# Kernel tuning notes

Hardware: AMD Instinct MI355X
Metric: run time of the kernel (lower is better)

## Reference

```python
import jax, jax.numpy as jnp
import numpy as np
from jax import lax

CIN, COUT, K, PAD = 256, 128, 3, 1


def setup_inputs() -> dict:
    key = jax.random.key(0)
    ks = jax.random.split(key, 5)
    N, h0, w0 = 2, 64, 64
    x = jax.random.normal(ks[0], (N, CIN, h0, w0), jnp.float32)
    lateral_feat = jax.random.normal(ks[1], (N, COUT, 1, 1), jnp.float32)
    trans_w = jax.random.normal(ks[2], (CIN, COUT, K, K), jnp.float32) * 0.02
    off_w1 = jax.random.normal(ks[3], (64, COUT, 3, 3), jnp.float32) * 0.02
    off_b1 = jnp.zeros((64,), jnp.float32)
    off_w2 = jax.random.normal(ks[4], (2 * K * K, 64, 3, 3), jnp.float32) * 0.02
    off_b2 = jnp.zeros((2 * K * K,), jnp.float32)
    return dict(x=x, lateral_feat=lateral_feat, trans_w=trans_w,
                off_w1=off_w1, off_b1=off_b1, off_w2=off_w2, off_b2=off_b2)


def _conv2d(x, w, b, pad):
    y = lax.conv_general_dilated(x, w, (1, 1), [(pad, pad), (pad, pad)],
                                 dimension_numbers=('NCHW', 'OIHW', 'NCHW'))
    return y + b[None, :, None, None]


def _conv_transpose2d(x, w, stride, pad, out_pad):
    # torch ConvTranspose2d weight layout: [Cin, Cout, k, k]
    k = w.shape[2]
    wt = jnp.flip(w, (2, 3)).transpose(1, 0, 2, 3)  # [Cout, Cin, k, k]
    lo = k - 1 - pad
    hi = k - 1 - pad + out_pad
    return lax.conv_general_dilated(x, wt, (1, 1), [(lo, hi), (lo, hi)],
                                    lhs_dilation=(stride, stride),
                                    dimension_numbers=('NCHW', 'OIHW', 'NCHW'))


def _deform_conv2d(x, offset, w, pad):
    # x [N,C,H,W], offset [N,2*K*K,H,W] (y,x interleaved per kernel tap), w [O,C,K,K]
    N, C, H, W = x.shape
    O = w.shape[0]
    KK = K * K
    off = offset.reshape(N, KK, 2, H, W)
    ky = jnp.arange(KK) // K
    kx = jnp.arange(KK) % K
    py = jnp.arange(H)[None, None, :, None] + (ky - pad)[None, :, None, None] + off[:, :, 0]
    px = jnp.arange(W)[None, None, None, :] + (kx - pad)[None, :, None, None] + off[:, :, 1]
    y0 = jnp.floor(py)
    x0 = jnp.floor(px)
    dy = py - y0
    dx = px - x0
    y0i = y0.astype(jnp.int32)
    x0i = x0.astype(jnp.int32)
    xf = x.reshape(N, C, H * W)

    def corner(yi, xi, wgt):
        valid = (yi >= 0) & (yi < H) & (xi >= 0) & (xi < W)
        idx = (jnp.clip(yi, 0, H - 1) * W + jnp.clip(xi, 0, W - 1)).reshape(N, -1)
        v = jnp.take_along_axis(xf, idx[:, None, :], axis=2).reshape(N, C, KK, H, W)
        return v * (wgt * valid)[:, None]

    sampled = (corner(y0i, x0i, (1 - dy) * (1 - dx))
               + corner(y0i, x0i + 1, (1 - dy) * dx)
               + corner(y0i + 1, x0i, dy * (1 - dx))
               + corner(y0i + 1, x0i + 1, dy * dx))  # [N,C,KK,H,W]
    return jnp.einsum('nckhw,ock->nohw', sampled, w.reshape(O, C, KK))


def reference(x, lateral_feat, trans_w, off_w1, off_b1, off_w2, off_b2):
    up = _conv_transpose2d(x, trans_w, 2, PAD, 1)          # [N, COUT, 2h0, 2w0]
    h = jax.nn.relu(_conv2d(lateral_feat, off_w1, off_b1, 1))
    offset = jnp.tanh(_conv2d(h, off_w2, off_b2, 1))       # [N, 18, 1, 1]
    N, C, H, W = up.shape
    # offset.repeat(1, 1, H, W) with 1x1 spatial input == broadcast to full grid
    offset = jnp.broadcast_to(offset, (N, 2 * K * K, H, W))
    # deform_conv2d uses trans_conv weight [O=CIN, I=COUT, K, K], stride=1, pad=PAD
    return _deform_conv2d(up, offset, trans_w, PAD)        # [N, CIN, H, W]
```

## Files before the change

### kernel.cpp

```cpp
#include <hip/hip_runtime.h>
#include <hip/hip_bf16.h>
#include <math.h>

typedef __attribute__((ext_vector_type(8))) short s16x8;
typedef __attribute__((ext_vector_type(4))) float f32x4;
typedef __attribute__((ext_vector_type(2))) float v2f;

__device__ __forceinline__ unsigned short f2bf(float f) {
    union { float f; unsigned int u; } v; v.f = f;
    unsigned int u = v.u + 0x7FFFu + ((v.u >> 16) & 1u);
    return (unsigned short)(u >> 16);
}
__device__ __forceinline__ unsigned pk2(float lo, float hi) {
    __hip_bfloat162 h = __float22bfloat162_rn(make_float2(lo, hi));
    union { __hip_bfloat162 h; unsigned u; } v; v.h = h;
    return v.u;
}
__device__ __forceinline__ v2f up2(unsigned u) {
    union { unsigned u; float f; } a, b;
    a.u = u << 16; b.u = u & 0xffff0000u;
    v2f r; r.x = a.f; r.y = b.f; return r;
}

__device__ __forceinline__ void blend4(uint4 uA, uint4 uB, uint4 uC, uint4 uD,
                                       v2f c00, v2f c01, v2f c10, v2f c11,
                                       unsigned short* dst) {
    unsigned ua[4] = {uA.x, uA.y, uA.z, uA.w};
    unsigned ub[4] = {uB.x, uB.y, uB.z, uB.w};
    unsigned uc[4] = {uC.x, uC.y, uC.z, uC.w};
    unsigned ud[4] = {uD.x, uD.y, uD.z, uD.w};
    unsigned pk[4];
#pragma unroll
    for (int i = 0; i < 4; ++i) {
        v2f r = c00 * up2(ua[i]) + c01 * up2(ub[i]) + c10 * up2(uc[i]) + c11 * up2(ud[i]);
        pk[i] = pk2(r.x, r.y);
    }
    *(uint4*)dst = make_uint4(pk[0], pk[1], pk[2], pk[3]);
}

__global__ __launch_bounds__(256) void k_prep(const float* __restrict__ x,
                                              const float* __restrict__ lat,
                                              const float* __restrict__ tw,
                                              const float* __restrict__ w1,
                                              const float* __restrict__ b1,
                                              const float* __restrict__ w2,
                                              const float* __restrict__ b2,
                                              unsigned short* __restrict__ xp,
                                              unsigned short* __restrict__ A2f,
                                              unsigned short* __restrict__ Awf,
                                              int* __restrict__ ipar,
                                              float* __restrict__ fpar) {
    __shared__ float sm[8420];
    int b = blockIdx.x, t = threadIdx.x;
    if (b == 0) {
        for (int i = t; i < 8192; i += 256) sm[(i >> 7) * 129 + (i & 127)] = w1[i * 9 + 4];
        __syncthreads();
        if (t < 128) {
            int n = t >> 6, o = t & 63;
            float s = b1[o];
            const float* ln = lat + n * 128;
#pragma unroll 8
            for (int c = 0; c < 128; ++c) s += ln[c] * sm[o * 129 + c];
            sm[8256 + t] = fmaxf(s, 0.f);
        }
        __syncthreads();
        if (t < 36) {
            int n = t / 18, j = t % 18;
            float s = b2[j];
            for (int o = 0; o < 64; ++o) s += sm[8256 + n * 64 + o] * w2[(j * 64 + o) * 9 + 4];
            float ov = tanhf(s);
            ov = fminf(fmaxf(ov, -0.999999f), 0.999999f);
            sm[8384 + t] = ov;
        }
        __syncthreads();
        if (t < 36) {
            int n = t / 18, j = t % 18;
            int tap = j >> 1, d = j & 1;
            float ov = sm[8384 + t];
            float fl = floorf(ov);
            int kc = d ? (tap % 3) : (tap / 3);
            ipar[(n * 9 + tap) * 2 + d] = kc - 1 + (int)fl;
            fpar[(n * 9 + tap) * 2 + d] = ov - fl;
        }
    } else if (b < 145) {
        int slot = (b - 1) * 256 + t;
        int l = slot & 63;
        int mi = (slot >> 6) & 3;
        int w = (slot >> 8) & 3;
        int k = slot >> 10;
        int row = w * 64 + mi * 16 + (l & 15);
        int kq = l >> 4;
        unsigned short v[8];
#pragma unroll
        for (int j = 0; j < 8; ++j) {
            int kcol = k * 32 + kq * 8 + j;
            int tap = kcol >> 7, c = kcol & 127;
            v[j] = f2bf(tw[(row * 128 + c) * 9 + tap]);
        }
        unsigned p0 = (unsigned)v[0] | ((unsigned)v[1] << 16);
        unsigned p1 = (unsigned)v[2] | ((unsigned)v[3] << 16);
        unsigned p2 = (unsigned)v[4] | ((unsigned)v[5] << 16);
        unsigned p3 = (unsigned)v[6] | ((unsigned)v[7] << 16);
        *(uint4*)(A2f + slot * 8) = make_uint4(p0, p1, p2, p3);
    } else if (b < 289) {
        int slot = (b - 145) * 256 + t;
        int l = slot & 63;
        int mi = (slot >> 6) & 3;
        int wm = (slot >> 8) & 1;
        int k = slot >> 9;
        int row = wm * 64 + mi * 16 + (l & 15);
        int kq = l >> 4;
        unsigned short v[8];
#pragma unroll
        for (int j = 0; j < 8; ++j) {
            int kcol = k * 32 + kq * 8 + j;
            int t9 = kcol >> 8, ci = kcol & 255;
            int ky = t9 / 3, kx = t9 - ky * 3;
            v[j] = f2bf(tw[(ci * 128 + row) * 9 + (2 - ky) * 3 + (2 - kx)]);
        }
        unsigned p0 = (unsigned)v[0] | ((unsigned)v[1] << 16);
        unsigned p1 = (unsigned)v[2] | ((unsigned)v[3] << 16);
        unsigned p2 = (unsigned)v[4] | ((unsigned)v[5] << 16);
        unsigned p3 = (unsigned)v[6] | ((unsigned)v[7] << 16);
        *(uint4*)(Awf + slot * 8) = make_uint4(p0, p1, p2, p3);
    } else {
        int bb = b - 289;
        int h = bb & 63, cq = (bb >> 6) & 3, n = bb >> 8;
        int c0 = cq * 64;
        {
            int wcol = t & 63, sub = t >> 6;
            for (int r = 0; r < 16; ++r) {
                int ci_l = r * 4 + sub;
                sm[ci_l * 65 + wcol] = x[((n * 256 + c0 + ci_l) * 64 + h) * 64 + wcol];
            }
        }
        __syncthreads();
        int wcol = t >> 2, cg = t & 3;
        unsigned short* dst = xp + (size_t)n * (65 * 65 * 256) + (h * 65 + wcol) * 256 + c0 + cg * 16;
        unsigned pk[8];
#pragma unroll
        for (int j = 0; j < 8; ++j)
            pk[j] = pk2(sm[(cg * 16 + 2 * j) * 65 + wcol], sm[(cg * 16 + 2 * j + 1) * 65 + wcol]);
        *(uint4*)dst = make_uint4(pk[0], pk[1], pk[2], pk[3]);
        *(uint4*)(dst + 8) = make_uint4(pk[4], pk[5], pk[6], pk[7]);
    }
}

__global__ __launch_bounds__(256) void k_tconv4(const unsigned short* __restrict__ xp,
                                                const unsigned short* __restrict__ Awf,
                                                unsigned short* __restrict__ upp) {
    int t = threadIdx.x;
    int b = blockIdx.x;
    int cls = b >> 7;
    int phase = (cls < 2) ? 1 : 0;
    int xpar = 1 - (cls & 1);
    int idx = b & 127;
    int n = idx >> 6, yh = idx & 63;
    int y = 2 * yh + phase;
    const unsigned short* xpn = xp + (size_t)n * (65 * 65 * 256);

    int lane = t & 63, w = t >> 6;
    int col = lane & 15, q = lane >> 4;
    int pos = w * 16 + col;

    int nky = phase ? 2 : 1;
    int nkx = xpar ? 2 : 1;

    f32x4 acc[8];
#pragma unroll
    for (int mi = 0; mi < 8; ++mi) acc[mi] = (f32x4){0.f, 0.f, 0.f, 0.f};

    const unsigned short* Afl = Awf + lane * 8;

    for (int a1 = 0; a1 < nky; ++a1) {
        int ky = phase ? (a1 ? 2 : 0) : 1;
        int d2 = (y + ky - 1) >> 1;
        for (int a2 = 0; a2 < nkx; ++a2) {
            int kx = xpar ? (a2 ? 2 : 0) : 1;
            int s = (xpar + kx - 1) >> 1;
            int t9 = ky * 3 + kx;
            const unsigned short* bptr = xpn + ((size_t)(d2 * 65 + s + pos)) * 256 + q * 8;
            const unsigned short* aptr = Afl + t9 * 8 * 4096;
#pragma unroll 2
            for (int cb = 0; cb < 8; ++cb) {
                s16x8 bf = *(const s16x8*)(bptr + cb * 32);
                s16x8 a[8];
#pragma unroll
                for (int mi = 0; mi < 8; ++mi)
                    a[mi] = *(const s16x8*)(aptr + cb * 4096 + (mi >> 2) * 2048 + (mi & 3) * 512);
#pragma unroll
                for (int mi = 0; mi < 8; ++mi)
                    acc[mi] = __builtin_amdgcn_mfma_f32_16x16x32_bf16(a[mi], bf, acc[mi], 0, 0, 0);
            }
        }
    }

    unsigned short* uppn = upp + (size_t)n * (132 * 132 * 128);
    int xg = 2 * pos + xpar;
#pragma unroll
    for (int mi = 0; mi < 8; ++mi) {
        int co = mi * 16 + q * 4;
        unsigned short* p = uppn + ((y + 2) * 132 + (xg + 2)) * 128 + co;
        unsigned lo = pk2(acc[mi][0], acc[mi][1]);
        unsigned hi = pk2(acc[mi][2], acc[mi][3]);
        *(uint2*)p = make_uint2(lo, hi);
    }
}

__global__ __launch_bounds__(256, 2) void k_deform4(const unsigned short* __restrict__ upp,
                                                    const unsigned short* __restrict__ A2f,
                                                    const int* __restrict__ ipar,
                                                    const float* __restrict__ fpar,
                                                    float* __restrict__ out) {
    __shared__ unsigned short Bs[2][64][84];
    int t = threadIdx.x;
    int b = blockIdx.x;
    int xcd = b & 7, j = b >> 3;
    int n = xcd >> 2, band = xcd & 3;
    int y = band * 32 + (j & 31);
    int tx0 = (j >> 5) * 64;
    const unsigned short* uppn = upp + (size_t)n * (132 * 132 * 128);

    int lane = t & 63, w = t >> 6;
    int col = lane & 15, q = lane >> 4;
    int bx = t >> 2, bcg = t & 3;
    int boff = bx * 128 + bcg * 8;

    const int* ipn = ipar + n * 18;
    const float* fpn = fpar + n * 18;

    f32x4 acc[4][4];
#pragma unroll
    for (int mi = 0; mi < 4; ++mi)
#pragma unroll
        for (int ni = 0; ni < 4; ++ni) acc[mi][ni] = (f32x4){0.f, 0.f, 0.f, 0.f};

    const unsigned short* Afw = A2f + w * 2048 + lane * 8;

#define TAPP(tap, PB, C00, C01, C10, C11)                                        \
    {                                                                            \
        int iy = ipn[(tap)*2], ix = ipn[(tap)*2 + 1];                            \
        float fy = fpn[(tap)*2], fx = fpn[(tap)*2 + 1];                          \
        float w00 = (1.f - fy) * (1.f - fx), w01 = (1.f - fy) * fx;              \
        float w10 = fy * (1.f - fx), w11 = fy * fx;                              \
        C00 = (v2f){w00, w00}; C01 = (v2f){w01, w01};                            \
        C10 = (v2f){w10, w10}; C11 = (v2f){w11, w11};                            \
        PB = uppn + ((size_t)((y + 2 + iy) * 132 + (tx0 + 2 + ix))) * 128 + boff;\
    }

    const unsigned short* pb;
    v2f cN00, cN01, cN10, cN11;
    uint4 cr[8];
    s16x8 a_cur[8], a_nxt[8];

    TAPP(0, pb, cN00, cN01, cN10, cN11);
#pragma unroll
    for (int c = 0; c < 2; ++c) {
        const unsigned short* p = pb + c * 32;
        cr[c * 4 + 0] = *(const uint4*)p;
        cr[c * 4 + 1] = *(const uint4*)(p + 128);
        cr[c * 4 + 2] = *(const uint4*)(p + 16896);
        cr[c * 4 + 3] = *(const uint4*)(p + 17024);
    }
#pragma unroll
    for (int c = 0; c < 2; ++c)
#pragma unroll
        for (int mi = 0; mi < 4; ++mi)
            a_cur[c * 4 + mi] = *(const s16x8*)(Afw + c * 8192 + mi * 512);
#pragma unroll
    for (int c = 0; c < 2; ++c)
        blend4(cr[c * 4 + 0], cr[c * 4 + 1], cr[c * 4 + 2], cr[c * 4 + 3],
               cN00, cN01, cN10, cN11, &Bs[0][bx][c * 42 + bcg * 8]);
#pragma unroll
    for (int c = 0; c < 2; ++c) {
        const unsigned short* p = pb + 64 + c * 32;
        cr[c * 4 + 0] = *(const uint4*)p;
        cr[c * 4 + 1] = *(const uint4*)(p + 128);
        cr[c * 4 + 2] = *(const uint4*)(p + 16896);
        cr[c * 4 + 3] = *(const uint4*)(p + 17024);
    }
    __syncthreads();

#pragma unroll 2
    for (int kk = 0; kk < 18; ++kk) {
        int cur = kk & 1;
        if (kk < 17) {
#pragma unroll
            for (int c = 0; c < 2; ++c)
                blend4(cr[c * 4 + 0], cr[c * 4 + 1], cr[c * 4 + 2], cr[c * 4 + 3],
                       cN00, cN01, cN10, cN11, &Bs[cur ^ 1][bx][c * 42 + bcg * 8]);
#pragma unroll
            for (int c = 0; c < 2; ++c)
#pragma unroll
                for (int mi = 0; mi < 4; ++mi)
                    a_nxt[c * 4 + mi] = *(const s16x8*)(Afw + (size_t)(2 * (kk + 1) + c) * 8192 + mi * 512);
        }
        if (kk < 16) {
            int kk2 = kk + 2;
            TAPP(kk2 >> 1, pb, cN00, cN01, cN10, cN11);
            int cb0 = (kk2 & 1) ? 64 : 0;
#pragma unroll
            for (int c = 0; c < 2; ++c) {
                const unsigned short* p = pb + cb0 + c * 32;
                cr[c * 4 + 0] = *(const uint4*)p;
                cr[c * 4 + 1] = *(const uint4*)(p + 128);
                cr[c * 4 + 2] = *(const uint4*)(p + 16896);
                cr[c * 4 + 3] = *(const uint4*)(p + 17024);
            }
        }
#pragma unroll
        for (int c = 0; c < 2; ++c) {
            s16x8 bbf[4];
#pragma unroll
            for (int ni = 0; ni < 4; ++ni)
                bbf[ni] = *(const s16x8*)&Bs[cur][ni * 16 + col][c * 42 + q * 8];
#pragma unroll
            for (int mi = 0; mi < 4; ++mi)
#pragma unroll
                for (int ni = 0; ni < 4; ++ni)
                    acc[mi][ni] = __builtin_amdgcn_mfma_f32_16x16x32_bf16(a_cur[c * 4 + mi], bbf[ni], acc[mi][ni], 0, 0, 0);
        }
        if (kk < 17) {
#pragma unroll
            for (int i = 0; i < 8; ++i) a_cur[i] = a_nxt[i];
        }
        __syncthreads();
    }
#undef TAPP

#pragma unroll
    for (int mi = 0; mi < 4; ++mi)
#pragma unroll
        for (int ni = 0; ni < 4; ++ni) {
            int o = w * 64 + mi * 16 + q * 4;
            int xg = tx0 + ni * 16 + col;
            float* p = out + (((size_t)(n * 256 + o)) * 128 + y) * 128 + xg;
            p[0]         = acc[mi][ni][0];
            p[16384]     = acc[mi][ni][1];
            p[2 * 16384] = acc[mi][ni][2];
            p[3 * 16384] = acc[mi][ni][3];
        }
}

extern "C" void kernel_launch(void* const* d_in, const int* in_sizes, int n_in,
                              void* d_out, int out_size, void* d_ws, size_t ws_size,
                              hipStream_t stream) {
    const float* x   = (const float*)d_in[0];
    const float* lat = (const float*)d_in[1];
    const float* tw  = (const float*)d_in[2];
    const float* w1  = (const float*)d_in[3];
    const float* b1  = (const float*)d_in[4];
    const float* w2  = (const float*)d_in[5];
    const float* b2  = (const float*)d_in[6];
    float* out = (float*)d_out;

    char* ws = (char*)d_ws;
    unsigned short* upp = (unsigned short*)ws;
    unsigned short* xp  = (unsigned short*)(ws + 8921088);
    unsigned short* A2f = (unsigned short*)(ws + 13247488);
    unsigned short* Awf = (unsigned short*)(ws + 13837312);
    int*   ipar         = (int*)(ws + 14427136);
    float* fpar         = (float*)(ws + 14427424);

    hipMemsetAsync(ws, 0, 13247488, stream);
    k_prep<<<801, 256, 0, stream>>>(x, lat, tw, w1, b1, w2, b2, xp, A2f, Awf, ipar, fpar);
    k_tconv4<<<512, 256, 0, stream>>>(xp, Awf, upp);
    k_deform4<<<512, 256, 0, stream>>>(upp, A2f, ipar, fpar, out);
}
```

Baseline: 157.9 us.

## Fold bilinear deform sampling into per-shift effective weights for the deform GEMM

Because the offsets are spatially uniform, the bilinear sampling is rewritten as a sum over a small set of unique integer shifts of the upsampled map. Each shift gets an effective weight matrix built by combining the per-tap weights with the bilinear coefficients in a new k_buildA kernel. The deform kernel then becomes a plain MFMA GEMM that loads B fragments directly from global memory, with no per-block blending or shared-memory staging and a dynamic K length. This adds a kernel launch and a larger workspace, and it relies on uniform offsets, which holds for the reference semantics.

```diff
diff --git a/kernel.cpp b/kernel.cpp
--- a/kernel.cpp
+++ b/kernel.cpp
@@ -20,22 +20,6 @@
     union { unsigned u; float f; } a, b;
     a.u = u << 16; b.u = u & 0xffff0000u;
     v2f r; r.x = a.f; r.y = b.f; return r;
-}
-
-__device__ __forceinline__ void blend4(uint4 uA, uint4 uB, uint4 uC, uint4 uD,
-                                       v2f c00, v2f c01, v2f c10, v2f c11,
-                                       unsigned short* dst) {
-    unsigned ua[4] = {uA.x, uA.y, uA.z, uA.w};
-    unsigned ub[4] = {uB.x, uB.y, uB.z, uB.w};
-    unsigned uc[4] = {uC.x, uC.y, uC.z, uC.w};
-    unsigned ud[4] = {uD.x, uD.y, uD.z, uD.w};
-    unsigned pk[4];
-#pragma unroll
-    for (int i = 0; i < 4; ++i) {
-        v2f r = c00 * up2(ua[i]) + c01 * up2(ub[i]) + c10 * up2(uc[i]) + c11 * up2(ud[i]);
-        pk[i] = pk2(r.x, r.y);
-    }
-    *(uint4*)dst = make_uint4(pk[0], pk[1], pk[2], pk[3]);
 }
 
 __global__ __launch_bounds__(256) void k_prep(const float* __restrict__ x,
@@ -46,11 +30,13 @@
                                               const float* __restrict__ w2,
                                               const float* __restrict__ b2,
                                               unsigned short* __restrict__ xp,
-                                              unsigned short* __restrict__ A2f,
+                                              unsigned short* __restrict__ A2,
                                               unsigned short* __restrict__ Awf,
-                                              int* __restrict__ ipar,
-                                              float* __restrict__ fpar) {
+                                              int* __restrict__ soff_g,
+                                              int* __restrict__ nsl_g,
+                                              float* __restrict__ weff_g) {
     __shared__ float sm[8420];
+    __shared__ int ish[200];
     int b = blockIdx.x, t = threadIdx.x;
     if (b == 0) {
         for (int i = t; i < 8192; i += 256) sm[(i >> 7) * 129 + (i & 127)] = w1[i * 9 + 4];
@@ -73,35 +59,67 @@
             sm[8384 + t] = ov;
         }
         __syncthreads();
-        if (t < 36) {
-            int n = t / 18, j = t % 18;
-            int tap = j >> 1, d = j & 1;
-            float ov = sm[8384 + t];
-            float fl = floorf(ov);
-            int kc = d ? (tap % 3) : (tap / 3);
-            ipar[(n * 9 + tap) * 2 + d] = kc - 1 + (int)fl;
-            fpar[(n * 9 + tap) * 2 + d] = ov - fl;
+        if (t < 2) {
+            int n2 = t;
+            float* wl = &sm[n2 * 256];
+            int* dyA  = &ish[n2 * 100];
+            int* dxA  = dyA + 25;
+            int* keyA = dyA + 50;
+            int* mapA = dyA + 75;
+            for (int i = 0; i < 225; ++i) wl[i] = 0.f;
+            for (int i = 0; i < 25; ++i) mapA[i] = -1;
+            int ns = 0;
+            for (int tap = 0; tap < 9; ++tap) {
+                float oy = sm[8384 + n2 * 18 + 2 * tap];
+                float ox = sm[8384 + n2 * 18 + 2 * tap + 1];
+                float fly = floorf(oy), flx = floorf(ox);
+                int iy = tap / 3 - 1 + (int)fly;
+                int ix = tap % 3 - 1 + (int)flx;
+                float fy = oy - fly, fx = ox - flx;
+                for (int cr = 0; cr < 4; ++cr) {
+                    int cy = cr >> 1, cx = cr & 1;
+                    float wv = (cy ? fy : 1.f - fy) * (cx ? fx : 1.f - fx);
+                    if (wv == 0.f) continue;
+                    int dy = iy + cy, dx = ix + cx;
+                    int sid = (dy + 2) * 5 + (dx + 2);
+                    int s = mapA[sid];
+                    if (s < 0) { s = ns; mapA[sid] = s; dyA[s] = dy; dxA[s] = dx; keyA[s] = sid; ++ns; }
+                    wl[s * 9 + tap] += wv;
+                }
+            }
+            for (int a = 0; a < ns - 1; ++a) {
+                int m = a;
+                for (int bq = a + 1; bq < ns; ++bq) if (keyA[bq] < keyA[m]) m = bq;
+                if (m != a) {
+                    int tmp;
+                    tmp = keyA[a]; keyA[a] = keyA[m]; keyA[m] = tmp;
+                    tmp = dyA[a];  dyA[a]  = dyA[m];  dyA[m]  = tmp;
+                    tmp = dxA[a];  dxA[a]  = dxA[m];  dxA[m]  = tmp;
+                    for (int e = 0; e < 9; ++e) {
+                        float f = wl[a * 9 + e]; wl[a * 9 + e] = wl[m * 9 + e]; wl[m * 9 + e] = f;
+                    }
+                }
+            }
+            nsl_g[n2] = ns * 4;
+            for (int s = 0; s < ns; ++s)
+                soff_g[n2 * 32 + s] = (dyA[s] * 132 + dxA[s]) * 128;
+            for (int i = 0; i < 225; ++i) weff_g[n2 * 225 + i] = wl[i];
         }
     } else if (b < 145) {
-        int slot = (b - 1) * 256 + t;
-        int l = slot & 63;
-        int mi = (slot >> 6) & 3;
-        int w = (slot >> 8) & 3;
-        int k = slot >> 10;
-        int row = w * 64 + mi * 16 + (l & 15);
-        int kq = l >> 4;
+        int e0 = ((b - 1) * 256 + t) * 8;
+        int o = e0 / 1152, rem = e0 - o * 1152;
         unsigned short v[8];
 #pragma unroll
-        for (int j = 0; j < 8; ++j) {
-            int kcol = k * 32 + kq * 8 + j;
-            int tap = kcol >> 7, c = kcol & 127;
-            v[j] = f2bf(tw[(row * 128 + c) * 9 + tap]);
+        for (int jj = 0; jj < 8; ++jj) {
+            int kk = rem + jj;
+            int tap = kk >> 7, c = kk & 127;
+            v[jj] = f2bf(tw[(o * 128 + c) * 9 + tap]);
         }
         unsigned p0 = (unsigned)v[0] | ((unsigned)v[1] << 16);
         unsigned p1 = (unsigned)v[2] | ((unsigned)v[3] << 16);
         unsigned p2 = (unsigned)v[4] | ((unsigned)v[5] << 16);
         unsigned p3 = (unsigned)v[6] | ((unsigned)v[7] << 16);
-        *(uint4*)(A2f + slot * 8) = make_uint4(p0, p1, p2, p3);
+        *(uint4*)(A2 + e0) = make_uint4(p0, p1, p2, p3);
     } else if (b < 289) {
         int slot = (b - 145) * 256 + t;
         int l = slot & 63;
@@ -112,11 +130,11 @@
         int kq = l >> 4;
         unsigned short v[8];
 #pragma unroll
-        for (int j = 0; j < 8; ++j) {
-            int kcol = k * 32 + kq * 8 + j;
+        for (int jj = 0; jj < 8; ++jj) {
+            int kcol = k * 32 + kq * 8 + jj;
             int t9 = kcol >> 8, ci = kcol & 255;
             int ky = t9 / 3, kx = t9 - ky * 3;
-            v[j] = f2bf(tw[(ci * 128 + row) * 9 + (2 - ky) * 3 + (2 - kx)]);
+            v[jj] = f2bf(tw[(ci * 128 + row) * 9 + (2 - ky) * 3 + (2 - kx)]);
         }
         unsigned p0 = (unsigned)v[0] | ((unsigned)v[1] << 16);
         unsigned p1 = (unsigned)v[2] | ((unsigned)v[3] << 16);
@@ -139,10 +157,50 @@
         unsigned short* dst = xp + (size_t)n * (65 * 65 * 256) + (h * 65 + wcol) * 256 + c0 + cg * 16;
         unsigned pk[8];
 #pragma unroll
-        for (int j = 0; j < 8; ++j)
-            pk[j] = pk2(sm[(cg * 16 + 2 * j) * 65 + wcol], sm[(cg * 16 + 2 * j + 1) * 65 + wcol]);
+        for (int jj = 0; jj < 8; ++jj)
+            pk[jj] = pk2(sm[(cg * 16 + 2 * jj) * 65 + wcol], sm[(cg * 16 + 2 * jj + 1) * 65 + wcol]);
         *(uint4*)dst = make_uint4(pk[0], pk[1], pk[2], pk[3]);
         *(uint4*)(dst + 8) = make_uint4(pk[4], pk[5], pk[6], pk[7]);
+    }
+}
+
+__global__ __launch_bounds__(256) void k_buildA(const unsigned short* __restrict__ A2,
+                                                const float* __restrict__ weff_g,
+                                                const int* __restrict__ nsl_g,
+                                                unsigned short* __restrict__ Apf) {
+    __shared__ float wt[9];
+    int b = blockIdx.x;
+    int n = b / 100, k = b % 100;
+    if (k >= nsl_g[n]) return;
+    int s = k >> 2, cq = k & 3;
+    int t = threadIdx.x;
+    if (t < 9) wt[t] = weff_g[n * 225 + s * 9 + t];
+    __syncthreads();
+    int w = t >> 6, mi = (t >> 4) & 3, lg = t & 15;
+#pragma unroll
+    for (int i = 0; i < 4; ++i) {
+        int l = lg * 4 + i;
+        int row = w * 64 + mi * 16 + (l & 15);
+        int kq = l >> 4;
+        int c0 = cq * 32 + kq * 8;
+        const unsigned short* ap = A2 + row * 1152 + c0;
+        v2f val[4] = {(v2f){0.f,0.f},(v2f){0.f,0.f},(v2f){0.f,0.f},(v2f){0.f,0.f}};
+#pragma unroll
+        for (int tap = 0; tap < 9; ++tap) {
+            float wv = wt[tap];
+            v2f wv2 = (v2f){wv, wv};
+            uint4 u = *(const uint4*)(ap + tap * 128);
+            val[0] += wv2 * up2(u.x);
+            val[1] += wv2 * up2(u.y);
+            val[2] += wv2 * up2(u.z);
+            val[3] += wv2 * up2(u.w);
+        }
+        uint4 o4;
+        o4.x = pk2(val[0].x, val[0].y);
+        o4.y = pk2(val[1].x, val[1].y);
+        o4.z = pk2(val[2].x, val[2].y);
+        o4.w = pk2(val[3].x, val[3].y);
+        *(uint4*)(Apf + (size_t)n * 819200 + ((((k * 4 + w) * 4 + mi) * 64 + l) * 8)) = o4;
     }
 }
 
@@ -207,12 +265,11 @@
     }
 }
 
-__global__ __launch_bounds__(256, 2) void k_deform4(const unsigned short* __restrict__ upp,
-                                                    const unsigned short* __restrict__ A2f,
-                                                    const int* __restrict__ ipar,
-                                                    const float* __restrict__ fpar,
-                                                    float* __restrict__ out) {
-    __shared__ unsigned short Bs[2][64][84];
+__global__ __launch_bounds__(256) void k_deform5(const unsigned short* __restrict__ upp,
+                                                 const unsigned short* __restrict__ Apf,
+                                                 const int* __restrict__ soff_g,
+                                                 const int* __restrict__ nsl_g,
+                                                 float* __restrict__ out) {
     int t = threadIdx.x;
     int b = blockIdx.x;
     int xcd = b & 7, j = b >> 3;
@@ -223,11 +280,11 @@
 
     int lane = t & 63, w = t >> 6;
     int col = lane & 15, q = lane >> 4;
-    int bx = t >> 2, bcg = t & 3;
-    int boff = bx * 128 + bcg * 8;
-
-    const int* ipn = ipar + n * 18;
-    const float* fpn = fpar + n * 18;
+
+    int nch = nsl_g[n];
+    const int* soff = soff_g + n * 32;
+    const unsigned short* Af = Apf + (size_t)n * 819200 + w * 2048 + lane * 8;
+    int bb = ((y + 2) * 132 + (tx0 + 2)) * 128 + q * 8;
 
     f32x4 acc[4][4];
 #pragma unroll
@@ -235,98 +292,39 @@
 #pragma unroll
         for (int ni = 0; ni < 4; ++ni) acc[mi][ni] = (f32x4){0.f, 0.f, 0.f, 0.f};
 
-    const unsigned short* Afw = A2f + w * 2048 + lane * 8;
-
-#define TAPP(tap, PB, C00, C01, C10, C11)                                        \
-    {                                                                            \
-        int iy = ipn[(tap)*2], ix = ipn[(tap)*2 + 1];                            \
-        float fy = fpn[(tap)*2], fx = fpn[(tap)*2 + 1];                          \
-        float w00 = (1.f - fy) * (1.f - fx), w01 = (1.f - fy) * fx;              \
-        float w10 = fy * (1.f - fx), w11 = fy * fx;                              \
-        C00 = (v2f){w00, w00}; C01 = (v2f){w01, w01};                            \
-        C10 = (v2f){w10, w10}; C11 = (v2f){w11, w11};                            \
-        PB = uppn + ((size_t)((y + 2 + iy) * 132 + (tx0 + 2 + ix))) * 128 + boff;\
-    }
-
-    const unsigned short* pb;
-    v2f cN00, cN01, cN10, cN11;
-    uint4 cr[8];
-    s16x8 a_cur[8], a_nxt[8];
-
-    TAPP(0, pb, cN00, cN01, cN10, cN11);
-#pragma unroll
-    for (int c = 0; c < 2; ++c) {
-        const unsigned short* p = pb + c * 32;
-        cr[c * 4 + 0] = *(const uint4*)p;
-        cr[c * 4 + 1] = *(const uint4*)(p + 128);
-        cr[c * 4 + 2] = *(const uint4*)(p + 16896);
-        cr[c * 4 + 3] = *(const uint4*)(p + 17024);
-    }
-#pragma unroll
-    for (int c = 0; c < 2; ++c)
+    s16x8 a_c[4], b_c[4], a_n[4], b_n[4];
+    {
+        const unsigned short* bp = uppn + bb + soff[0];
+#pragma unroll
+        for (int ni = 0; ni < 4; ++ni)
+            b_c[ni] = *(const s16x8*)(bp + (ni * 16 + col) * 128);
 #pragma unroll
         for (int mi = 0; mi < 4; ++mi)
-            a_cur[c * 4 + mi] = *(const s16x8*)(Afw + c * 8192 + mi * 512);
-#pragma unroll
-    for (int c = 0; c < 2; ++c)
-        blend4(cr[c * 4 + 0], cr[c * 4 + 1], cr[c * 4 + 2], cr[c * 4 + 3],
-               cN00, cN01, cN10, cN11, &Bs[0][bx][c * 42 + bcg * 8]);
-#pragma unroll
-    for (int c = 0; c < 2; ++c) {
-        const unsigned short* p = pb + 64 + c * 32;
-        cr[c * 4 + 0] = *(const uint4*)p;
-        cr[c * 4 + 1] = *(const uint4*)(p + 128);
-        cr[c * 4 + 2] = *(const uint4*)(p + 16896);
-        cr[c * 4 + 3] = *(const uint4*)(p + 17024);
-    }
-    __syncthreads();
+            a_c[mi] = *(const s16x8*)(Af + mi * 512);
+    }
 
 #pragma unroll 2
-    for (int kk = 0; kk < 18; ++kk) {
-        int cur = kk & 1;
-        if (kk < 17) {
-#pragma unroll
-            for (int c = 0; c < 2; ++c)
-                blend4(cr[c * 4 + 0], cr[c * 4 + 1], cr[c * 4 + 2], cr[c * 4 + 3],
-                       cN00, cN01, cN10, cN11, &Bs[cur ^ 1][bx][c * 42 + bcg * 8]);
-#pragma unroll
-            for (int c = 0; c < 2; ++c)
-#pragma unroll
-                for (int mi = 0; mi < 4; ++mi)
-                    a_nxt[c * 4 + mi] = *(const s16x8*)(Afw + (size_t)(2 * (kk + 1) + c) * 8192 + mi * 512);
-        }
-        if (kk < 16) {
-            int kk2 = kk + 2;
-            TAPP(kk2 >> 1, pb, cN00, cN01, cN10, cN11);
-            int cb0 = (kk2 & 1) ? 64 : 0;
-#pragma unroll
-            for (int c = 0; c < 2; ++c) {
-                const unsigned short* p = pb + cb0 + c * 32;
-                cr[c * 4 + 0] = *(const uint4*)p;
-                cr[c * 4 + 1] = *(const uint4*)(p + 128);
-                cr[c * 4 + 2] = *(const uint4*)(p + 16896);
-                cr[c * 4 + 3] = *(const uint4*)(p + 17024);
-            }
-        }
-#pragma unroll
-        for (int c = 0; c < 2; ++c) {
-            s16x8 bbf[4];
+    for (int k = 0; k < nch; ++k) {
+        int k1 = k + 1;
+        if (k1 < nch) {
+            const unsigned short* bp = uppn + bb + soff[k1 >> 2] + (k1 & 3) * 32;
 #pragma unroll
             for (int ni = 0; ni < 4; ++ni)
-                bbf[ni] = *(const s16x8*)&Bs[cur][ni * 16 + col][c * 42 + q * 8];
+                b_n[ni] = *(const s16x8*)(bp + (ni * 16 + col) * 128);
 #pragma unroll
             for (int mi = 0; mi < 4; ++mi)
-#pragma unroll
-                for (int ni = 0; ni < 4; ++ni)
-                    acc[mi][ni] = __builtin_amdgcn_mfma_f32_16x16x32_bf16(a_cur[c * 4 + mi], bbf[ni], acc[mi][ni], 0, 0, 0);
-        }
-        if (kk < 17) {
-#pragma unroll
-            for (int i = 0; i < 8; ++i) a_cur[i] = a_nxt[i];
-        }
-        __syncthreads();
-    }
-#undef TAPP
+                a_n[mi] = *(const s16x8*)(Af + k1 * 8192 + mi * 512);
+        }
+#pragma unroll
+        for (int mi = 0; mi < 4; ++mi)
+#pragma unroll
+            for (int ni = 0; ni < 4; ++ni)
+                acc[mi][ni] = __builtin_amdgcn_mfma_f32_16x16x32_bf16(a_c[mi], b_c[ni], acc[mi][ni], 0, 0, 0);
+        if (k1 < nch) {
+#pragma unroll
+            for (int i = 0; i < 4; ++i) { a_c[i] = a_n[i]; b_c[i] = b_n[i]; }
+        }
+    }
 
 #pragma unroll
     for (int mi = 0; mi < 4; ++mi)
@@ -355,15 +353,18 @@
     float* out = (float*)d_out;
 
     char* ws = (char*)d_ws;
-    unsigned short* upp = (unsigned short*)ws;
-    unsigned short* xp  = (unsigned short*)(ws + 8921088);
-    unsigned short* A2f = (unsigned short*)(ws + 13247488);
-    unsigned short* Awf = (unsigned short*)(ws + 13837312);
-    int*   ipar         = (int*)(ws + 14427136);
-    float* fpar         = (float*)(ws + 14427424);
+    unsigned short* upp  = (unsigned short*)ws;
+    unsigned short* xp   = (unsigned short*)(ws + 8921088);
+    unsigned short* Awf  = (unsigned short*)(ws + 13247488);
+    unsigned short* A2   = (unsigned short*)(ws + 13837312);
+    unsigned short* Apf  = (unsigned short*)(ws + 14427136);
+    int*   soff          = (int*)(ws + 17703936);
+    int*   nsl           = (int*)(ws + 17704192);
+    float* weff          = (float*)(ws + 17704200);
 
     hipMemsetAsync(ws, 0, 13247488, stream);
-    k_prep<<<801, 256, 0, stream>>>(x, lat, tw, w1, b1, w2, b2, xp, A2f, Awf, ipar, fpar);
+    k_prep<<<801, 256, 0, stream>>>(x, lat, tw, w1, b1, w2, b2, xp, A2, Awf, soff, nsl, weff);
+    k_buildA<<<200, 256, 0, stream>>>(A2, weff, nsl, Apf);
     k_tconv4<<<512, 256, 0, stream>>>(xp, Awf, upp);
-    k_deform4<<<512, 256, 0, stream>>>(upp, A2f, ipar, fpar, out);
-}
+    k_deform5<<<512, 256, 0, stream>>>(upp, Apf, soff, nsl, out);
+}
```

After: 251.4 us. 1.59x slower.

## Split deform GEMM across 8 waves per block and stage tap params in LDS

Applied to the files above, without the earlier changes.

The deform kernel moves from 4 to 8 waves per block. The 64-pixel N dimension is split across two wave groups, which halves each wave's accumulator tile and the per-thread gather/blend work. Tap base offsets and bilinear weights are precomputed once into shared memory instead of being recomputed per thread, and the A-fragment prefetch is restructured into even/odd halves to cut register pressure. The aim is higher occupancy and better latency hiding for the gathers. The cost is that each weight fragment is now loaded by twice as many waves and more threads take part in each barrier.

```diff
diff --git a/kernel.cpp b/kernel.cpp
--- a/kernel.cpp
+++ b/kernel.cpp
@@ -23,8 +23,9 @@
 }
 
 __device__ __forceinline__ void blend4(uint4 uA, uint4 uB, uint4 uC, uint4 uD,
-                                       v2f c00, v2f c01, v2f c10, v2f c11,
-                                       unsigned short* dst) {
+                                       float4 cw, unsigned short* dst) {
+    v2f c00 = (v2f){cw.x, cw.x}, c01 = (v2f){cw.y, cw.y};
+    v2f c10 = (v2f){cw.z, cw.z}, c11 = (v2f){cw.w, cw.w};
     unsigned ua[4] = {uA.x, uA.y, uA.z, uA.w};
     unsigned ub[4] = {uB.x, uB.y, uB.z, uB.w};
     unsigned uc[4] = {uC.x, uC.y, uC.z, uC.w};
@@ -207,12 +208,14 @@
     }
 }
 
-__global__ __launch_bounds__(256, 2) void k_deform4(const unsigned short* __restrict__ upp,
+__global__ __launch_bounds__(512, 4) void k_deform6(const unsigned short* __restrict__ upp,
                                                     const unsigned short* __restrict__ A2f,
                                                     const int* __restrict__ ipar,
                                                     const float* __restrict__ fpar,
                                                     float* __restrict__ out) {
     __shared__ unsigned short Bs[2][64][84];
+    __shared__ int sbase[9];
+    __shared__ float4 swt[9];
     int t = threadIdx.x;
     int b = blockIdx.x;
     int xcd = b & 7, j = b >> 3;
@@ -222,118 +225,106 @@
     const unsigned short* uppn = upp + (size_t)n * (132 * 132 * 128);
 
     int lane = t & 63, w = t >> 6;
+    int wm = w & 3, wn = w >> 2;
     int col = lane & 15, q = lane >> 4;
-    int bx = t >> 2, bcg = t & 3;
-    int boff = bx * 128 + bcg * 8;
-
-    const int* ipn = ipar + n * 18;
-    const float* fpn = fpar + n * 18;
-
-    f32x4 acc[4][4];
+    int bx = t >> 3, sub = t & 7;
+    int cst = sub >> 2, bcg = sub & 3;
+    int boff = bx * 128 + cst * 32 + bcg * 8;
+
+    if (t < 9) {
+        int iy = ipar[(n * 9 + t) * 2 + 0], ix = ipar[(n * 9 + t) * 2 + 1];
+        float fy = fpar[(n * 9 + t) * 2 + 0], fx = fpar[(n * 9 + t) * 2 + 1];
+        sbase[t] = ((y + 2 + iy) * 132 + (tx0 + 2 + ix)) * 128;
+        swt[t] = make_float4((1.f - fy) * (1.f - fx), (1.f - fy) * fx, fy * (1.f - fx), fy * fx);
+    }
+
+    f32x4 acc[4][2];
 #pragma unroll
     for (int mi = 0; mi < 4; ++mi)
 #pragma unroll
-        for (int ni = 0; ni < 4; ++ni) acc[mi][ni] = (f32x4){0.f, 0.f, 0.f, 0.f};
-
-    const unsigned short* Afw = A2f + w * 2048 + lane * 8;
-
-#define TAPP(tap, PB, C00, C01, C10, C11)                                        \
-    {                                                                            \
-        int iy = ipn[(tap)*2], ix = ipn[(tap)*2 + 1];                            \
-        float fy = fpn[(tap)*2], fx = fpn[(tap)*2 + 1];                          \
-        float w00 = (1.f - fy) * (1.f - fx), w01 = (1.f - fy) * fx;              \
-        float w10 = fy * (1.f - fx), w11 = fy * fx;                              \
-        C00 = (v2f){w00, w00}; C01 = (v2f){w01, w01};                            \
-        C10 = (v2f){w10, w10}; C11 = (v2f){w11, w11};                            \
-        PB = uppn + ((size_t)((y + 2 + iy) * 132 + (tx0 + 2 + ix))) * 128 + boff;\
-    }
-
-    const unsigned short* pb;
-    v2f cN00, cN01, cN10, cN11;
-    uint4 cr[8];
-    s16x8 a_cur[8], a_nxt[8];
-
-    TAPP(0, pb, cN00, cN01, cN10, cN11);
-#pragma unroll
-    for (int c = 0; c < 2; ++c) {
-        const unsigned short* p = pb + c * 32;
-        cr[c * 4 + 0] = *(const uint4*)p;
-        cr[c * 4 + 1] = *(const uint4*)(p + 128);
-        cr[c * 4 + 2] = *(const uint4*)(p + 16896);
-        cr[c * 4 + 3] = *(const uint4*)(p + 17024);
-    }
-#pragma unroll
-    for (int c = 0; c < 2; ++c)
+        for (int ni = 0; ni < 2; ++ni) acc[mi][ni] = (f32x4){0.f, 0.f, 0.f, 0.f};
+
+    __syncthreads();
+
+    const unsigned short* Afw = A2f + wm * 2048 + lane * 8;
+    s16x8 a_ev[4], a_od[4];
+    uint4 cA, cB, cC, cD;
+    float4 cwp;
+
+    {
+        const unsigned short* p = uppn + sbase[0] + boff;
+        uint4 uA = *(const uint4*)p;
+        uint4 uB = *(const uint4*)(p + 128);
+        uint4 uC = *(const uint4*)(p + 16896);
+        uint4 uD = *(const uint4*)(p + 17024);
+        blend4(uA, uB, uC, uD, swt[0], &Bs[0][bx][cst * 42 + bcg * 8]);
+        const unsigned short* p2 = p + 64;
+        cA = *(const uint4*)p2;
+        cB = *(const uint4*)(p2 + 128);
+        cC = *(const uint4*)(p2 + 16896);
+        cD = *(const uint4*)(p2 + 17024);
+        cwp = swt[0];
 #pragma unroll
         for (int mi = 0; mi < 4; ++mi)
-            a_cur[c * 4 + mi] = *(const s16x8*)(Afw + c * 8192 + mi * 512);
-#pragma unroll
-    for (int c = 0; c < 2; ++c)
-        blend4(cr[c * 4 + 0], cr[c * 4 + 1], cr[c * 4 + 2], cr[c * 4 + 3],
-               cN00, cN01, cN10, cN11, &Bs[0][bx][c * 42 + bcg * 8]);
-#pragma unroll
-    for (int c = 0; c < 2; ++c) {
-        const unsigned short* p = pb + 64 + c * 32;
-        cr[c * 4 + 0] = *(const uint4*)p;
-        cr[c * 4 + 1] = *(const uint4*)(p + 128);
-        cr[c * 4 + 2] = *(const uint4*)(p + 16896);
-        cr[c * 4 + 3] = *(const uint4*)(p + 17024);
+            a_ev[mi] = *(const s16x8*)(Afw + mi * 512);
     }
     __syncthreads();
 
-#pragma unroll 2
     for (int kk = 0; kk < 18; ++kk) {
         int cur = kk & 1;
-        if (kk < 17) {
-#pragma unroll
-            for (int c = 0; c < 2; ++c)
-                blend4(cr[c * 4 + 0], cr[c * 4 + 1], cr[c * 4 + 2], cr[c * 4 + 3],
-                       cN00, cN01, cN10, cN11, &Bs[cur ^ 1][bx][c * 42 + bcg * 8]);
-#pragma unroll
-            for (int c = 0; c < 2; ++c)
+        if (kk < 17)
+            blend4(cA, cB, cC, cD, cwp, &Bs[cur ^ 1][bx][cst * 42 + bcg * 8]);
+        if (kk < 16) {
+            int k2 = kk + 2;
+            int tap2 = k2 >> 1, cb0 = (k2 & 1) * 64;
+            cwp = swt[tap2];
+            const unsigned short* p = uppn + sbase[tap2] + cb0 + boff;
+            cA = *(const uint4*)p;
+            cB = *(const uint4*)(p + 128);
+            cC = *(const uint4*)(p + 16896);
+            cD = *(const uint4*)(p + 17024);
+        }
+        {
+            int nc = 2 * kk + 1;
+#pragma unroll
+            for (int mi = 0; mi < 4; ++mi)
+                a_od[mi] = *(const s16x8*)(Afw + nc * 8192 + mi * 512);
+            s16x8 bf[2];
+#pragma unroll
+            for (int ni = 0; ni < 2; ++ni)
+                bf[ni] = *(const s16x8*)&Bs[cur][wn * 32 + ni * 16 + col][q * 8];
+#pragma unroll
+            for (int mi = 0; mi < 4; ++mi)
+#pragma unroll
+                for (int ni = 0; ni < 2; ++ni)
+                    acc[mi][ni] = __builtin_amdgcn_mfma_f32_16x16x32_bf16(a_ev[mi], bf[ni], acc[mi][ni], 0, 0, 0);
+        }
+        {
+            if (kk < 17) {
+                int nc = 2 * (kk + 1);
 #pragma unroll
                 for (int mi = 0; mi < 4; ++mi)
-                    a_nxt[c * 4 + mi] = *(const s16x8*)(Afw + (size_t)(2 * (kk + 1) + c) * 8192 + mi * 512);
-        }
-        if (kk < 16) {
-            int kk2 = kk + 2;
-            TAPP(kk2 >> 1, pb, cN00, cN01, cN10, cN11);
-            int cb0 = (kk2 & 1) ? 64 : 0;
-#pragma unroll
-            for (int c = 0; c < 2; ++c) {
-                const unsigned short* p = pb + cb0 + c * 32;
-                cr[c * 4 + 0] = *(const uint4*)p;
-                cr[c * 4 + 1] = *(const uint4*)(p + 128);
-                cr[c * 4 + 2] = *(const uint4*)(p + 16896);
-                cr[c * 4 + 3] = *(const uint4*)(p + 17024);
+                    a_ev[mi] = *(const s16x8*)(Afw + nc * 8192 + mi * 512);
             }
-        }
-#pragma unroll
-        for (int c = 0; c < 2; ++c) {
-            s16x8 bbf[4];
-#pragma unroll
-            for (int ni = 0; ni < 4; ++ni)
-                bbf[ni] = *(const s16x8*)&Bs[cur][ni * 16 + col][c * 42 + q * 8];
+            s16x8 bf[2];
+#pragma unroll
+            for (int ni = 0; ni < 2; ++ni)
+                bf[ni] = *(const s16x8*)&Bs[cur][wn * 32 + ni * 16 + col][42 + q * 8];
 #pragma unroll
             for (int mi = 0; mi < 4; ++mi)
 #pragma unroll
-                for (int ni = 0; ni < 4; ++ni)
-                    acc[mi][ni] = __builtin_amdgcn_mfma_f32_16x16x32_bf16(a_cur[c * 4 + mi], bbf[ni], acc[mi][ni], 0, 0, 0);
-        }
-        if (kk < 17) {
-#pragma unroll
-            for (int i = 0; i < 8; ++i) a_cur[i] = a_nxt[i];
-        }
-        __syncthreads();
-    }
-#undef TAPP
+                for (int ni = 0; ni < 2; ++ni)
+                    acc[mi][ni] = __builtin_amdgcn_mfma_f32_16x16x32_bf16(a_od[mi], bf[ni], acc[mi][ni], 0, 0, 0);
+        }
+        __syncthreads();
+    }
 
 #pragma unroll
     for (int mi = 0; mi < 4; ++mi)
 #pragma unroll
-        for (int ni = 0; ni < 4; ++ni) {
-            int o = w * 64 + mi * 16 + q * 4;
-            int xg = tx0 + ni * 16 + col;
+        for (int ni = 0; ni < 2; ++ni) {
+            int o = wm * 64 + mi * 16 + q * 4;
+            int xg = tx0 + wn * 32 + ni * 16 + col;
             float* p = out + (((size_t)(n * 256 + o)) * 128 + y) * 128 + xg;
             p[0]         = acc[mi][ni][0];
             p[16384]     = acc[mi][ni][1];
@@ -365,5 +356,5 @@
     hipMemsetAsync(ws, 0, 13247488, stream);
     k_prep<<<801, 256, 0, stream>>>(x, lat, tw, w1, b1, w2, b2, xp, A2f, Awf, ipar, fpar);
     k_tconv4<<<512, 256, 0, stream>>>(xp, Awf, upp);
-    k_deform4<<<512, 256, 0, stream>>>(upp, A2f, ipar, fpar, out);
-}
+    k_deform6<<<512, 512, 0, stream>>>(upp, A2f, ipar, fpar, out);
+}
```

New measurement: 160.3 us. No clear change (+1.5%).
